# Optimization experiments

Hardware: AMD Instinct MI355X
Metric: run time of the kernel (lower is better)

Reference implementation:

```python
import jax, jax.numpy as jnp
import numpy as np

B, S, D = 4, 2048, 1024
H = 16
HD = D // H  # 64


def setup_inputs() -> dict:
    key = jax.random.key(0)
    ks = jax.random.split(key, 5)
    std = 1.0 / np.sqrt(D)
    return {
        "x": jax.random.normal(ks[0], (B, S, D), dtype=jnp.float32),
        "Wq": jax.random.normal(ks[1], (D, D), dtype=jnp.float32) * std,
        "Wk": jax.random.normal(ks[2], (D, D), dtype=jnp.float32) * std,
        "Wv": jax.random.normal(ks[3], (D, D), dtype=jnp.float32) * std,
        "Wo": jax.random.normal(ks[4], (D, D), dtype=jnp.float32) * std,
        "bo": jnp.zeros((D,), dtype=jnp.float32),
    }


def reference(x, Wq, Wk, Wv, Wo, bo):
    b, n, d_in = x.shape
    q = (x @ Wq).reshape(b, n, H, HD).transpose(0, 2, 1, 3)  # [b,h,n,hd]
    k = (x @ Wk).reshape(b, n, H, HD).transpose(0, 2, 1, 3)
    v = (x @ Wv).reshape(b, n, H, HD).transpose(0, 2, 1, 3)
    scores = jnp.einsum("bhqd,bhkd->bhqk", q, k)  # full NxN, as in original
    causal = jnp.tril(jnp.ones((n, n), dtype=bool))  # True = keep
    scores = jnp.where(causal, scores, -jnp.inf)
    attn = jax.nn.softmax(scores / np.sqrt(HD), axis=-1)
    # dropout p=0.0 -> identity
    ctx = jnp.einsum("bhqk,bhkd->bqhd", attn, v).reshape(b, n, H * HD)
    return ctx @ Wo + bo
```

## Files before the change

kernel.cpp:

```cpp
#include <hip/hip_runtime.h>
#include <math.h>

#define BATCH 4
#define SLEN 2048
#define DMODEL 1024
#define NH 16
#define HD 64
#define MROWS (BATCH * SLEN)
#define QK_LD 2048

typedef __attribute__((ext_vector_type(8))) short short8;
typedef __attribute__((ext_vector_type(4))) float floatx4;

#define AS1 __attribute__((address_space(1)))
#define AS3 __attribute__((address_space(3)))

__device__ inline unsigned short f2bf(float f) {
    union { float f; unsigned u; } a; a.f = f;
    unsigned r = a.u + 0x7fff + ((a.u >> 16) & 1);
    return (unsigned short)(r >> 16);
}

__device__ inline unsigned pack_bf(float lo, float hi) {
    union { float f; unsigned u; } a, b; a.f = lo; b.f = hi;
    return __builtin_amdgcn_perm(b.u + 0x8000u, a.u + 0x8000u, 0x07060302u);
}
__device__ inline unsigned pack_tr(float lo, float hi) {
    union { float f; unsigned u; } a, b; a.f = lo; b.f = hi;
    return __builtin_amdgcn_perm(b.u, a.u, 0x07060302u);
}


__global__ __launch_bounds__(256) void cvt_bf16(const float* __restrict__ src,
                                                short* __restrict__ dst) {
    int i = (blockIdx.x * 256 + threadIdx.x) * 4;
    float4 v = *(const float4*)(src + i);
    unsigned short t0 = f2bf(v.x), t1 = f2bf(v.y), t2 = f2bf(v.z), t3 = f2bf(v.w);
    uint2 o;
    o.x = (unsigned)t0 | ((unsigned)t1 << 16);
    o.y = (unsigned)t2 | ((unsigned)t3 << 16);
    *(uint2*)(dst + i) = o;
}

__global__ __launch_bounds__(256) void cvt_wT4(
    const float* __restrict__ Wq, const float* __restrict__ Wk,
    const float* __restrict__ Wv, const float* __restrict__ Wo,
    short* __restrict__ WqkT, short* __restrict__ WvT, short* __restrict__ WoT)
{
    const float* W; short* Wt; float sc = 1.0f;
    int z = blockIdx.z;
    if (z == 0)      { W = Wq; Wt = WqkT; sc = 0.18033688011112042f; }
    else if (z == 1) { W = Wk; Wt = WqkT + (size_t)DMODEL * DMODEL; }
    else if (z == 2) { W = Wv; Wt = WvT; }
    else             { W = Wo; Wt = WoT; }

    __shared__ float t[32][33];
    int bn = blockIdx.x * 32, bk = blockIdx.y * 32;
    int tx = threadIdx.x & 31, r0 = (threadIdx.x >> 5) * 4;
    #pragma unroll
    for (int i = 0; i < 4; i++)
        t[r0 + i][tx] = W[(size_t)(bk + r0 + i) * DMODEL + bn + tx];
    __syncthreads();
    #pragma unroll
    for (int i = 0; i < 4; i++)
        Wt[(size_t)(bn + r0 + i) * DMODEL + bk + tx] = (short)f2bf(t[tx][r0 + i] * sc);
}

#define TM 128
#define TN 128
#define TK 32

template <int OUT_BF16>
__global__ __launch_bounds__(256) void mfma_gemm(
    const short* __restrict__ A,
    const short* __restrict__ Bt,
    const float* __restrict__ bias,
    void* __restrict__ Cout, int M, int N, int K)
{
    __shared__ short As[TM * TK];
    __shared__ short Bs[TN * TK];
    int tid = threadIdx.x;
    int m0 = blockIdx.y * TM, n0 = blockIdx.x * TN;
    int l = tid & 63, w = tid >> 6;
    int wm = (w >> 1) * 64, wn = (w & 1) * 64;
    int lr = l & 15, lk = (l >> 4) * 8;

    floatx4 acc[4][4] = {};

    for (int k0 = 0; k0 < K; k0 += TK) {
        #pragma unroll
        for (int r = 0; r < 2; r++) {
            int c = r * 256 + tid;
            int mm = c >> 2, kk = (c & 3) * 8;
            __builtin_amdgcn_global_load_lds(
                (const AS1 void*)(A + (size_t)(m0 + mm) * K + k0 + kk),
                (AS3 void*)(As + c * 8), 16, 0, 0);
            __builtin_amdgcn_global_load_lds(
                (const AS1 void*)(Bt + (size_t)(n0 + mm) * K + k0 + kk),
                (AS3 void*)(Bs + c * 8), 16, 0, 0);
        }
        __syncthreads();

        short8 af[4], bg[4];
        #pragma unroll
        for (int i = 0; i < 4; i++) {
            af[i] = *(const short8*)(As + (wm + i * 16 + lr) * TK + lk);
            bg[i] = *(const short8*)(Bs + (wn + i * 16 + lr) * TK + lk);
        }
        #pragma unroll
        for (int mi = 0; mi < 4; mi++)
            #pragma unroll
            for (int ni = 0; ni < 4; ni++)
                acc[mi][ni] = __builtin_amdgcn_mfma_f32_16x16x32_bf16(
                    af[mi], bg[ni], acc[mi][ni], 0, 0, 0);
        __syncthreads();
    }

    int rbase = (l >> 4) * 4, cbase = l & 15;
    if (OUT_BF16) {
        short* C = (short*)Cout;
        #pragma unroll
        for (int mi = 0; mi < 4; mi++)
            #pragma unroll
            for (int r = 0; r < 4; r++) {
                int row = m0 + wm + mi * 16 + rbase + r;
                #pragma unroll
                for (int ni = 0; ni < 4; ni++) {
                    int col = n0 + wn + ni * 16 + cbase;
                    C[(size_t)row * N + col] = (short)f2bf(acc[mi][ni][r]);
                }
            }
    } else {
        float* C = (float*)Cout;
        #pragma unroll
        for (int mi = 0; mi < 4; mi++)
            #pragma unroll
            for (int r = 0; r < 4; r++) {
                int row = m0 + wm + mi * 16 + rbase + r;
                #pragma unroll
                for (int ni = 0; ni < 4; ni++) {
                    int col = n0 + wn + ni * 16 + cbase;
                    C[(size_t)row * N + col] = acc[mi][ni][r] + bias[col];
                }
            }
    }
}

#define PSTR 72

__global__ __launch_bounds__(256) void fa_mfma(
    const short* __restrict__ QK, const short* __restrict__ VtT,
    short* __restrict__ ctx)
{
    __shared__ __align__(16) short Ks[2][64][32];
    __shared__ __align__(16) short Vs[2][64][32];
    __shared__ __align__(16) short Ps[4][16][PSTR];

    int tid = threadIdx.x;
    int l = tid & 63, w = tid >> 6;
    int lr = l & 15, lg = l >> 4;
    int bh = blockIdx.x;
    int b = bh >> 4, h = bh & 15;
    int p = blockIdx.y;

    const short* Qbase = QK + (size_t)b * SLEN * QK_LD + h * HD;
    const short* Kbase = Qbase + 1024;
    const short* Vbase = VtT + (size_t)h * HD * MROWS + b * SLEN;

    int xoff = (lg ^ ((lr >> 1) & 3)) * 8;

    short8 ones;
    #pragma unroll
    for (int j = 0; j < 8; j++) ones[j] = (short)0x3F80;

    #pragma unroll 1
    for (int half = 0; half < 2; half++) {
        int qt = (half == 0) ? (31 - p) : p;
        int q0 = qt * 64;
        int qrow = q0 + w * 16 + lr;

        short8 qf[2];
        #pragma unroll
        for (int kk = 0; kk < 2; kk++)
            qf[kk] = *(const short8*)(Qbase + (size_t)qrow * QK_LD + kk * 32 + lg * 8);

        floatx4 O[4] = {};
        floatx4 accL = {};

        for (int kt = 0; kt <= qt; kt++) {
            int k0 = kt * 64;
            __syncthreads();
            #pragma unroll
            for (int r2 = 0; r2 < 2; r2++) {
                int c = r2 * 256 + tid;
                int kh = c >> 8, rr = (c >> 2) & 63;
                int q = (c & 3) ^ ((rr >> 1) & 3);
                __builtin_amdgcn_global_load_lds(
                    (const AS1 void*)(Kbase + (size_t)(k0 + rr) * QK_LD + kh * 32 + q * 8),
                    (AS3 void*)(&Ks[0][0][0] + c * 8), 16, 0, 0);
                __builtin_amdgcn_global_load_lds(
                    (const AS1 void*)(Vbase + (size_t)rr * MROWS + k0 + kh * 32 + q * 8),
                    (AS3 void*)(&Vs[0][0][0] + c * 8), 16, 0, 0);
            }
            __syncthreads();

            floatx4 s4[4] = {};
            #pragma unroll
            for (int kk = 0; kk < 2; kk++)
                #pragma unroll
                for (int t = 0; t < 4; t++) {
                    short8 kf = *(const short8*)(&Ks[kk][t * 16 + lr][xoff]);
                    s4[t] = __builtin_amdgcn_mfma_f32_16x16x32_bf16(kf, qf[kk], s4[t], 0, 0, 0);
                }

            if (kt == qt) {
                #pragma unroll
                for (int t = 0; t < 4; t++)
                    #pragma unroll
                    for (int r = 0; r < 4; r++)
                        if (k0 + t * 16 + lg * 4 + r > qrow) s4[t][r] = -INFINITY;
            }

            #pragma unroll
            for (int t = 0; t < 4; t++) {
                float p0 = exp2f(s4[t][0]);
                float p1 = exp2f(s4[t][1]);
                float p2 = exp2f(s4[t][2]);
                float p3 = exp2f(s4[t][3]);
                uint2 pk;
                pk.x = pack_tr(p0, p1);
                pk.y = pack_tr(p2, p3);
                *(uint2*)(&Ps[w][lr][t * 16 + lg * 4]) = pk;
            }

            #pragma unroll
            for (int kk = 0; kk < 2; kk++) {
                short8 pf = *(const short8*)(&Ps[w][lr][kk * 32 + lg * 8]);
                accL = __builtin_amdgcn_mfma_f32_16x16x32_bf16(ones, pf, accL, 0, 0, 0);
                #pragma unroll
                for (int dt = 0; dt < 4; dt++) {
                    short8 vf = *(const short8*)(&Vs[kk][dt * 16 + lr][xoff]);
                    O[dt] = __builtin_amdgcn_mfma_f32_16x16x32_bf16(vf, pf, O[dt], 0, 0, 0);
                }
            }
        }

        float linv = 1.f / accL[0];
        short* crow = ctx + ((size_t)b * SLEN + qrow) * DMODEL + h * HD;
        #pragma unroll
        for (int dt = 0; dt < 4; dt++) {
            uint2 pk;
            pk.x = pack_bf(O[dt][0] * linv, O[dt][1] * linv);
            pk.y = pack_bf(O[dt][2] * linv, O[dt][3] * linv);
            *(uint2*)(crow + dt * 16 + lg * 4) = pk;
        }
    }
}

extern "C" void kernel_launch(void* const* d_in, const int* in_sizes, int n_in,
                              void* d_out, int out_size, void* d_ws, size_t ws_size,
                              hipStream_t stream) {
    const float* x  = (const float*)d_in[0];
    const float* Wq = (const float*)d_in[1];
    const float* Wk = (const float*)d_in[2];
    const float* Wv = (const float*)d_in[3];
    const float* Wo = (const float*)d_in[4];
    const float* bo = (const float*)d_in[5];
    float* out = (float*)d_out;

    const size_t tsz = (size_t)MROWS * DMODEL;
    const size_t wsz = (size_t)DMODEL * DMODEL;

    short* xb    = (short*)d_ws;
    short* WqkT  = xb + tsz;
    short* WvT   = WqkT + 2 * wsz;
    short* WoT   = WvT + wsz;
    short* QKb   = WoT + wsz;
    short* VtT   = QKb + 2 * tsz;
    short* Cb    = VtT + tsz;

    cvt_bf16<<<(int)(tsz / (256 * 4)), 256, 0, stream>>>(x, xb);
    cvt_wT4<<<dim3(32, 32, 4), 256, 0, stream>>>(Wq, Wk, Wv, Wo, WqkT, WvT, WoT);

    mfma_gemm<1><<<dim3(2048 / TN, MROWS / TM), 256, 0, stream>>>(
        xb, WqkT, nullptr, QKb, MROWS, 2048, DMODEL);
    mfma_gemm<1><<<dim3(MROWS / TN, DMODEL / TM), 256, 0, stream>>>(
        WvT, xb, nullptr, VtT, DMODEL, MROWS, DMODEL);

    fa_mfma<<<dim3(BATCH * NH, 16), 256, 0, stream>>>(QKb, VtT, Cb);

    mfma_gemm<0><<<dim3(DMODEL / TN, MROWS / TM), 256, 0, stream>>>(
        Cb, WoT, bo, out, MROWS, DMODEL, DMODEL);
}
```

Baseline: 291.5 us.

## Give each flash-attention block one query tile instead of a paired tile

The attention kernel drops the load-balancing scheme in which each block handled two query tiles (31-p and p). It now launches 32 tiles per batch-head, one block each, heaviest tiles first, which doubles the grid so more blocks can run concurrently. The change also adds a min-blocks-per-CU launch bound, switches to the raw hardware exp2 builtin, and computes K/V source pointers once and advances them each iteration instead of recomputing addresses. Blocks now carry uneven work and rely on the hardware scheduler to balance it, and the launch bound may force register spills.

```diff
diff --git a/kernel.cpp b/kernel.cpp
--- a/kernel.cpp
+++ b/kernel.cpp
@@ -148,7 +148,7 @@
 
 #define PSTR 72
 
-__global__ __launch_bounds__(256) void fa_mfma(
+__global__ __launch_bounds__(256, 4) void fa_mfma(
     const short* __restrict__ QK, const short* __restrict__ VtT,
     short* __restrict__ ctx)
 {
@@ -161,7 +161,8 @@
     int lr = l & 15, lg = l >> 4;
     int bh = blockIdx.x;
     int b = bh >> 4, h = bh & 15;
-    int p = blockIdx.y;
+    int qt = 31 - blockIdx.y;
+    int q0 = qt * 64;
 
     const short* Qbase = QK + (size_t)b * SLEN * QK_LD + h * HD;
     const short* Kbase = Qbase + 1024;
@@ -173,87 +174,93 @@
     #pragma unroll
     for (int j = 0; j < 8; j++) ones[j] = (short)0x3F80;
 
-    #pragma unroll 1
-    for (int half = 0; half < 2; half++) {
-        int qt = (half == 0) ? (31 - p) : p;
-        int q0 = qt * 64;
-        int qrow = q0 + w * 16 + lr;
-
-        short8 qf[2];
+    int qrow = q0 + w * 16 + lr;
+
+    short8 qf[2];
+    #pragma unroll
+    for (int kk = 0; kk < 2; kk++)
+        qf[kk] = *(const short8*)(Qbase + (size_t)qrow * QK_LD + kk * 32 + lg * 8);
+
+    const short* ksrc[2];
+    const short* vsrc[2];
+    #pragma unroll
+    for (int r2 = 0; r2 < 2; r2++) {
+        int cc = r2 * 256 + tid;
+        int kh = cc >> 8, rr = (cc >> 2) & 63;
+        int q = (cc & 3) ^ ((rr >> 1) & 3);
+        ksrc[r2] = Kbase + (size_t)rr * QK_LD + kh * 32 + q * 8;
+        vsrc[r2] = Vbase + (size_t)rr * MROWS + kh * 32 + q * 8;
+    }
+
+    floatx4 O[4] = {};
+    floatx4 accL = {};
+
+    for (int kt = 0; kt <= qt; kt++) {
+        int k0 = kt * 64;
+        __syncthreads();
+        #pragma unroll
+        for (int r2 = 0; r2 < 2; r2++) {
+            int cc = r2 * 256 + tid;
+            __builtin_amdgcn_global_load_lds(
+                (const AS1 void*)ksrc[r2],
+                (AS3 void*)(&Ks[0][0][0] + cc * 8), 16, 0, 0);
+            __builtin_amdgcn_global_load_lds(
+                (const AS1 void*)vsrc[r2],
+                (AS3 void*)(&Vs[0][0][0] + cc * 8), 16, 0, 0);
+            ksrc[r2] += (size_t)64 * QK_LD;
+            vsrc[r2] += 64;
+        }
+        __syncthreads();
+
+        floatx4 s4[4] = {};
         #pragma unroll
         for (int kk = 0; kk < 2; kk++)
-            qf[kk] = *(const short8*)(Qbase + (size_t)qrow * QK_LD + kk * 32 + lg * 8);
-
-        floatx4 O[4] = {};
-        floatx4 accL = {};
-
-        for (int kt = 0; kt <= qt; kt++) {
-            int k0 = kt * 64;
-            __syncthreads();
-            #pragma unroll
-            for (int r2 = 0; r2 < 2; r2++) {
-                int c = r2 * 256 + tid;
-                int kh = c >> 8, rr = (c >> 2) & 63;
-                int q = (c & 3) ^ ((rr >> 1) & 3);
-                __builtin_amdgcn_global_load_lds(
-                    (const AS1 void*)(Kbase + (size_t)(k0 + rr) * QK_LD + kh * 32 + q * 8),
-                    (AS3 void*)(&Ks[0][0][0] + c * 8), 16, 0, 0);
-                __builtin_amdgcn_global_load_lds(
-                    (const AS1 void*)(Vbase + (size_t)rr * MROWS + k0 + kh * 32 + q * 8),
-                    (AS3 void*)(&Vs[0][0][0] + c * 8), 16, 0, 0);
+            #pragma unroll
+            for (int t = 0; t < 4; t++) {
+                short8 kf = *(const short8*)(&Ks[kk][t * 16 + lr][xoff]);
+                s4[t] = __builtin_amdgcn_mfma_f32_16x16x32_bf16(kf, qf[kk], s4[t], 0, 0, 0);
             }
-            __syncthreads();
-
-            floatx4 s4[4] = {};
-            #pragma unroll
-            for (int kk = 0; kk < 2; kk++)
+
+        if (kt == qt) {
+            #pragma unroll
+            for (int t = 0; t < 4; t++)
                 #pragma unroll
-                for (int t = 0; t < 4; t++) {
-                    short8 kf = *(const short8*)(&Ks[kk][t * 16 + lr][xoff]);
-                    s4[t] = __builtin_amdgcn_mfma_f32_16x16x32_bf16(kf, qf[kk], s4[t], 0, 0, 0);
-                }
-
-            if (kt == qt) {
-                #pragma unroll
-                for (int t = 0; t < 4; t++)
-                    #pragma unroll
-                    for (int r = 0; r < 4; r++)
-                        if (k0 + t * 16 + lg * 4 + r > qrow) s4[t][r] = -INFINITY;
+                for (int r = 0; r < 4; r++)
+                    if (k0 + t * 16 + lg * 4 + r > qrow) s4[t][r] = -INFINITY;
+        }
+
+        #pragma unroll
+        for (int t = 0; t < 4; t++) {
+            float p0 = __builtin_amdgcn_exp2f(s4[t][0]);
+            float p1 = __builtin_amdgcn_exp2f(s4[t][1]);
+            float p2 = __builtin_amdgcn_exp2f(s4[t][2]);
+            float p3 = __builtin_amdgcn_exp2f(s4[t][3]);
+            uint2 pk;
+            pk.x = pack_tr(p0, p1);
+            pk.y = pack_tr(p2, p3);
+            *(uint2*)(&Ps[w][lr][t * 16 + lg * 4]) = pk;
+        }
+
+        #pragma unroll
+        for (int kk = 0; kk < 2; kk++) {
+            short8 pf = *(const short8*)(&Ps[w][lr][kk * 32 + lg * 8]);
+            accL = __builtin_amdgcn_mfma_f32_16x16x32_bf16(ones, pf, accL, 0, 0, 0);
+            #pragma unroll
+            for (int dt = 0; dt < 4; dt++) {
+                short8 vf = *(const short8*)(&Vs[kk][dt * 16 + lr][xoff]);
+                O[dt] = __builtin_amdgcn_mfma_f32_16x16x32_bf16(vf, pf, O[dt], 0, 0, 0);
             }
-
-            #pragma unroll
-            for (int t = 0; t < 4; t++) {
-                float p0 = exp2f(s4[t][0]);
-                float p1 = exp2f(s4[t][1]);
-                float p2 = exp2f(s4[t][2]);
-                float p3 = exp2f(s4[t][3]);
-                uint2 pk;
-                pk.x = pack_tr(p0, p1);
-                pk.y = pack_tr(p2, p3);
-                *(uint2*)(&Ps[w][lr][t * 16 + lg * 4]) = pk;
-            }
-
-            #pragma unroll
-            for (int kk = 0; kk < 2; kk++) {
-                short8 pf = *(const short8*)(&Ps[w][lr][kk * 32 + lg * 8]);
-                accL = __builtin_amdgcn_mfma_f32_16x16x32_bf16(ones, pf, accL, 0, 0, 0);
-                #pragma unroll
-                for (int dt = 0; dt < 4; dt++) {
-                    short8 vf = *(const short8*)(&Vs[kk][dt * 16 + lr][xoff]);
-                    O[dt] = __builtin_amdgcn_mfma_f32_16x16x32_bf16(vf, pf, O[dt], 0, 0, 0);
-                }
-            }
-        }
-
-        float linv = 1.f / accL[0];
-        short* crow = ctx + ((size_t)b * SLEN + qrow) * DMODEL + h * HD;
-        #pragma unroll
-        for (int dt = 0; dt < 4; dt++) {
-            uint2 pk;
-            pk.x = pack_bf(O[dt][0] * linv, O[dt][1] * linv);
-            pk.y = pack_bf(O[dt][2] * linv, O[dt][3] * linv);
-            *(uint2*)(crow + dt * 16 + lg * 4) = pk;
-        }
+        }
+    }
+
+    float linv = 1.f / accL[0];
+    short* crow = ctx + ((size_t)b * SLEN + qrow) * DMODEL + h * HD;
+    #pragma unroll
+    for (int dt = 0; dt < 4; dt++) {
+        uint2 pk;
+        pk.x = pack_bf(O[dt][0] * linv, O[dt][1] * linv);
+        pk.y = pack_bf(O[dt][2] * linv, O[dt][3] * linv);
+        *(uint2*)(crow + dt * 16 + lg * 4) = pk;
     }
 }
 
@@ -287,7 +294,7 @@
     mfma_gemm<1><<<dim3(MROWS / TN, DMODEL / TM), 256, 0, stream>>>(
         WvT, xb, nullptr, VtT, DMODEL, MROWS, DMODEL);
 
-    fa_mfma<<<dim3(BATCH * NH, 16), 256, 0, stream>>>(QKb, VtT, Cb);
+    fa_mfma<<<dim3(BATCH * NH, 32), 256, 0, stream>>>(QKb, VtT, Cb);
 
     mfma_gemm<0><<<dim3(DMODEL / TN, MROWS / TM), 256, 0, stream>>>(
         Cb, WoT, bo, out, MROWS, DMODEL, DMODEL);
```

Result: faster. 267.0 us (-8.4%).
